# Optimization experiments

Hardware: AMD Instinct MI355X
Metric: run time of the kernel (lower is better)

Reference implementation:

```python
import jax, jax.numpy as jnp
import numpy as np

WS = 7          # window_size
DIM = 256
H = 8           # num_heads
HD = DIM // H   # head_dim = 32
NW = 64         # windows per image
B = 64          # batch of images
B_ = B * NW
M_ = WS * WS + 1  # 50 tokens (cls + patches)


def _relative_position_index():
    coords = np.stack(np.meshgrid(np.arange(WS), np.arange(WS), indexing='ij'))  # (2, ws, ws)
    flat = coords.reshape(2, -1)  # (2, ws*ws)
    rel = flat[:, :, None] - flat[:, None, :]  # (2, N, N)
    rel = rel.transpose(1, 2, 0).astype(np.int64)
    rel[:, :, 0] += WS - 1
    rel[:, :, 1] += WS - 1
    rel[:, :, 0] *= 2 * WS - 1
    return rel.sum(-1).astype(np.int32)  # (N, N) in [0, (2ws-1)^2)


def setup_inputs() -> dict:
    key = jax.random.key(0)
    k1, k2, k3 = jax.random.split(key, 3)
    qkv = jax.random.normal(k1, (B_, M_, 3 * DIM), dtype=jnp.float32)
    mask = jax.random.normal(k2, (NW, M_ - 1, M_), dtype=jnp.float32)
    bias_table = jax.random.normal(k3, ((2 * WS - 1) ** 2, H), dtype=jnp.float32) * 0.02
    rel_index = jnp.asarray(_relative_position_index())
    return {"qkv": qkv, "mask": mask, "bias_table": bias_table, "rel_index": rel_index}


def reference(qkv, mask, bias_table, rel_index):
    Bw, M, C = qkv.shape
    scale = HD ** -0.5
    # (3, B_, H, M, hd)
    qkv = qkv.reshape(Bw, M, 3, H, HD).transpose(2, 0, 3, 1, 4)
    q = qkv[0][:, :, 1:, :] * scale   # queries drop cls token: (B_, H, M-1, hd)
    k, v = qkv[1], qkv[2]             # (B_, H, M, hd)
    attn = jnp.einsum('bhqd,bhkd->bhqk', q, k)  # (B_, H, M-1, M)
    # relative position bias over patch-patch block only
    N = WS * WS
    bias = bias_table[rel_index.reshape(-1)].reshape(N, N, H).transpose(2, 0, 1)  # (H, N, N)
    attn = jnp.concatenate([attn[..., :1], attn[..., 1:] + bias[None]], axis=-1)
    # additive window mask
    nW = mask.shape[0]
    attn = attn.reshape(Bw // nW, nW, H, M - 1, M) + mask[None, :, None]
    attn = jax.nn.softmax(attn.reshape(Bw, H, M - 1, M), axis=-1)
    x = jnp.einsum('bhqk,bhkd->bqhd', attn, v).reshape(Bw, M - 1, DIM)
    return x
```

## Files before the change

kernel.cpp:

```cpp
#include <hip/hip_runtime.h>
#include <stdint.h>

#define NQ 49
#define MT 50
#define NH 8
#define HD 32
#define NW 64
#define BWIN 4096
#define M2TOT (NW*NH*NQ*MT)

typedef __attribute__((ext_vector_type(8))) short short8;
typedef __attribute__((ext_vector_type(4))) float f32x4;

__device__ __forceinline__ uint32_t f2u(float x){ union{float f;uint32_t u;}c; c.f=x; return c.u; }
__device__ __forceinline__ float u2f(uint32_t u){ union{float f;uint32_t u;}c; c.u=u; return c.f; }
__device__ __forceinline__ uint32_t bf16rn(float x){
  uint32_t u = f2u(x);
  return (u + 0x7fffu + ((u >> 16) & 1u)) >> 16;
}
__device__ __forceinline__ void bsplit(float x, uint32_t& hi, uint32_t& lo){
  hi = bf16rn(x);
  lo = bf16rn(x - u2f(hi << 16));
}

__global__ void fuse_mb(const float* __restrict__ mask,
                        const float* __restrict__ bias_table,
                        const int*   __restrict__ rel_index,
                        float* __restrict__ M2)
{
  int idx = blockIdx.x * 256 + threadIdx.x;
  if (idx >= M2TOT) return;
  int j  = idx % MT;
  int t  = idx / MT;
  int i  = t % NQ;
  int t2 = t / NQ;
  int h  = t2 % NH;
  int w  = t2 / NH;
  float v = mask[(w * NQ + i) * MT + j];
  if (j > 0) v += bias_table[rel_index[i * NQ + (j - 1)] * NH + h];
  M2[idx] = v;
}

__global__ __launch_bounds__(128, 4)
void winattn_kernel(const float* __restrict__ qkv,
                    const float* __restrict__ M2,
                    float* __restrict__ out)
{
  __shared__ unsigned short sP[2][64 * 64];

  const int wv   = threadIdx.x >> 6;
  const int lane = threadIdx.x & 63;
  const int ln   = lane & 15;
  const int qd   = lane >> 4;

  const int id = blockIdx.x;
  const int b  = id >> 2;
  const int h  = ((id & 3) << 1) | wv;
  const int w  = b & (NW - 1);

  const float* base = qkv + (size_t)b * (MT * 3 * 256);
  const float scale = 0.17677669529663687f;

  short8 qh[4], ql[4], kh[4], kl[4];
#pragma unroll
  for (int t = 0; t < 4; ++t) {
    int m   = 16 * t + ln;
    int tok = (m < NQ ? m : NQ - 1) + 1;
    const float* p = base + (size_t)tok * 768 + h * HD + qd * 8;
    f32x4 e0 = *(const f32x4*)p;
    f32x4 e1 = *(const f32x4*)(p + 4);
#pragma unroll
    for (int j = 0; j < 8; ++j) {
      float x = (j < 4 ? e0[j] : e1[j - 4]) * scale;
      uint32_t hi, lo; bsplit(x, hi, lo);
      qh[t][j] = (short)(unsigned short)hi;
      ql[t][j] = (short)(unsigned short)lo;
    }
  }
#pragma unroll
  for (int u = 0; u < 4; ++u) {
    int n    = 16 * u + ln;
    int ktok = (n < MT ? n : MT - 1);
    const float* p = base + (size_t)ktok * 768 + 256 + h * HD + qd * 8;
    f32x4 e0 = *(const f32x4*)p;
    f32x4 e1 = *(const f32x4*)(p + 4);
#pragma unroll
    for (int j = 0; j < 8; ++j) {
      float x = (j < 4 ? e0[j] : e1[j - 4]);
      uint32_t hi, lo; bsplit(x, hi, lo);
      kh[u][j] = (short)(unsigned short)hi;
      kl[u][j] = (short)(unsigned short)lo;
    }
  }

  f32x4 S[4][4];
#pragma unroll
  for (int t = 0; t < 4; ++t) {
#pragma unroll
    for (int u = 0; u < 4; ++u) {
      f32x4 a = {0.f, 0.f, 0.f, 0.f};
      a = __builtin_amdgcn_mfma_f32_16x16x32_bf16(qh[t], kh[u], a, 0, 0, 0);
      a = __builtin_amdgcn_mfma_f32_16x16x32_bf16(qh[t], kl[u], a, 0, 0, 0);
      a = __builtin_amdgcn_mfma_f32_16x16x32_bf16(ql[t], kh[u], a, 0, 0, 0);
      S[t][u] = a;
    }
  }

  const float* mrow = M2 + ((size_t)(w * NH + h) * NQ) * MT;
#pragma unroll
  for (int t = 0; t < 4; ++t) {
#pragma unroll
    for (int r = 0; r < 4; ++r) {
      int i = 16 * t + 4 * qd + r;
#pragma unroll
      for (int u = 0; u < 4; ++u) {
        int j = 16 * u + ln;
        if (j >= MT)      S[t][u][r] = -1e30f;
        else if (i < NQ)  S[t][u][r] += mrow[i * MT + j];
      }
    }
  }

  float rsumv[4][4];
#pragma unroll
  for (int t = 0; t < 4; ++t) {
#pragma unroll
    for (int r = 0; r < 4; ++r) {
      float mx = fmaxf(fmaxf(S[t][0][r], S[t][1][r]), fmaxf(S[t][2][r], S[t][3][r]));
#pragma unroll
      for (int s = 1; s < 16; s <<= 1) mx = fmaxf(mx, __shfl_xor(mx, s, 16));
      int m  = 16 * t + 4 * qd + r;
      int m7 = m & 7;
      float sum = 0.f;
#pragma unroll
      for (int u = 0; u < 4; ++u) {
        float p = exp2f((S[t][u][r] - mx) * 1.4426950408889634f);
        sum += p;
        int c = 16 * u + ln;
        int addr = m * 64 + ((((c >> 3) ^ m7) << 3) | (c & 7));
        sP[wv][addr] = (unsigned short)bf16rn(p);
      }
#pragma unroll
      for (int s = 1; s < 16; s <<= 1) sum += __shfl_xor(sum, s, 16);
      rsumv[t][r] = sum;
    }
  }
  __syncthreads();

  short8 vh[2][2], vl[2][2];
#pragma unroll
  for (int kt = 0; kt < 2; ++kt) {
#pragma unroll
    for (int u2 = 0; u2 < 2; ++u2) {
#pragma unroll
      for (int j = 0; j < 8; ++j) {
        int k  = 32 * kt + 8 * qd + j;
        int d  = 16 * u2 + ln;
        int kc = (k < MT ? k : MT - 1);
        float x = base[(size_t)kc * 768 + 512 + h * HD + d];
        if (k >= MT) x = 0.f;
        uint32_t hi, lo; bsplit(x, hi, lo);
        vh[kt][u2][j] = (short)(unsigned short)hi;
        vl[kt][u2][j] = (short)(unsigned short)lo;
      }
    }
  }

  f32x4 O[4][2];
#pragma unroll
  for (int t = 0; t < 4; ++t)
#pragma unroll
    for (int u2 = 0; u2 < 2; ++u2) O[t][u2] = (f32x4){0.f, 0.f, 0.f, 0.f};

#pragma unroll
  for (int kt = 0; kt < 2; ++kt) {
#pragma unroll
    for (int t = 0; t < 4; ++t) {
      int m = 16 * t + ln;
      int phys = ((4 * kt + qd) ^ (ln & 7));
      short8 ph = *(const short8*)&sP[wv][m * 64 + (phys << 3)];
#pragma unroll
      for (int u2 = 0; u2 < 2; ++u2) {
        f32x4 a = O[t][u2];
        a = __builtin_amdgcn_mfma_f32_16x16x32_bf16(ph, vh[kt][u2], a, 0, 0, 0);
        a = __builtin_amdgcn_mfma_f32_16x16x32_bf16(ph, vl[kt][u2], a, 0, 0, 0);
        O[t][u2] = a;
      }
    }
  }

#pragma unroll
  for (int t = 0; t < 4; ++t) {
#pragma unroll
    for (int r = 0; r < 4; ++r) {
      int row = 16 * t + 4 * qd + r;
      if (row >= NQ) continue;
      float inv = 1.0f / rsumv[t][r];
#pragma unroll
      for (int u2 = 0; u2 < 2; ++u2) {
        int d = 16 * u2 + ln;
        out[(((size_t)b * NQ + row) * NH + h) * HD + d] = O[t][u2][r] * inv;
      }
    }
  }
}

extern "C" void kernel_launch(void* const* d_in, const int* in_sizes, int n_in,
                              void* d_out, int out_size, void* d_ws, size_t ws_size,
                              hipStream_t stream) {
  (void)in_sizes; (void)n_in; (void)ws_size; (void)out_size;
  const float* qkv        = (const float*)d_in[0];
  const float* mask       = (const float*)d_in[1];
  const float* bias_table = (const float*)d_in[2];
  const int*   rel_index  = (const int*)d_in[3];
  float* out = (float*)d_out;
  float* M2  = (float*)d_ws;

  fuse_mb<<<(M2TOT + 255) / 256, 256, 0, stream>>>(mask, bias_table, rel_index, M2);
  winattn_kernel<<<BWIN * 4, 128, 0, stream>>>(qkv, M2, out);
}
```

Baseline: 944.6 us.

## Fuse mask+bias precompute into attention kernel and stream Q tiles per row block

Drops the separate fuse_mb kernel and its M2 workspace. The attention kernel now reads the mask and gathers the relative-position bias directly through rel_index and bias_table. Q tiles are loaded and split per row block inside the score loop, which cuts live registers for Q and S. The hi part of the bf16 split now truncates instead of rounding. This removes a launch and the M2 write/read traffic, but adds an indirect gather per score element and changes the split rounding slightly.

```diff
diff --git a/kernel.cpp b/kernel.cpp
--- a/kernel.cpp
+++ b/kernel.cpp
@@ -7,7 +7,6 @@
 #define HD 32
 #define NW 64
 #define BWIN 4096
-#define M2TOT (NW*NH*NQ*MT)
 
 typedef __attribute__((ext_vector_type(8))) short short8;
 typedef __attribute__((ext_vector_type(4))) float f32x4;
@@ -19,31 +18,16 @@
   return (u + 0x7fffu + ((u >> 16) & 1u)) >> 16;
 }
 __device__ __forceinline__ void bsplit(float x, uint32_t& hi, uint32_t& lo){
-  hi = bf16rn(x);
-  lo = bf16rn(x - u2f(hi << 16));
-}
-
-__global__ void fuse_mb(const float* __restrict__ mask,
-                        const float* __restrict__ bias_table,
-                        const int*   __restrict__ rel_index,
-                        float* __restrict__ M2)
-{
-  int idx = blockIdx.x * 256 + threadIdx.x;
-  if (idx >= M2TOT) return;
-  int j  = idx % MT;
-  int t  = idx / MT;
-  int i  = t % NQ;
-  int t2 = t / NQ;
-  int h  = t2 % NH;
-  int w  = t2 / NH;
-  float v = mask[(w * NQ + i) * MT + j];
-  if (j > 0) v += bias_table[rel_index[i * NQ + (j - 1)] * NH + h];
-  M2[idx] = v;
+  uint32_t u = f2u(x);
+  hi = u >> 16;
+  lo = bf16rn(x - u2f(u & 0xffff0000u));
 }
 
 __global__ __launch_bounds__(128, 4)
 void winattn_kernel(const float* __restrict__ qkv,
-                    const float* __restrict__ M2,
+                    const float* __restrict__ mask,
+                    const float* __restrict__ bias_table,
+                    const int*   __restrict__ rel_index,
                     float* __restrict__ out)
 {
   __shared__ unsigned short sP[2][64 * 64];
@@ -61,22 +45,7 @@
   const float* base = qkv + (size_t)b * (MT * 3 * 256);
   const float scale = 0.17677669529663687f;
 
-  short8 qh[4], ql[4], kh[4], kl[4];
-#pragma unroll
-  for (int t = 0; t < 4; ++t) {
-    int m   = 16 * t + ln;
-    int tok = (m < NQ ? m : NQ - 1) + 1;
-    const float* p = base + (size_t)tok * 768 + h * HD + qd * 8;
-    f32x4 e0 = *(const f32x4*)p;
-    f32x4 e1 = *(const f32x4*)(p + 4);
-#pragma unroll
-    for (int j = 0; j < 8; ++j) {
-      float x = (j < 4 ? e0[j] : e1[j - 4]) * scale;
-      uint32_t hi, lo; bsplit(x, hi, lo);
-      qh[t][j] = (short)(unsigned short)hi;
-      ql[t][j] = (short)(unsigned short)lo;
-    }
-  }
+  short8 kh[4], kl[4];
 #pragma unroll
   for (int u = 0; u < 4; ++u) {
     int n    = 16 * u + ln;
@@ -93,52 +62,61 @@
     }
   }
 
-  f32x4 S[4][4];
+  const float* mrow = mask + (size_t)w * NQ * MT;
+  float rsumv[4][4];
+
 #pragma unroll
   for (int t = 0; t < 4; ++t) {
+    int m   = 16 * t + ln;
+    int tok = (m < NQ ? m : NQ - 1) + 1;
+    const float* p = base + (size_t)tok * 768 + h * HD + qd * 8;
+    f32x4 e0 = *(const f32x4*)p;
+    f32x4 e1 = *(const f32x4*)(p + 4);
+    short8 qh, ql;
+#pragma unroll
+    for (int j = 0; j < 8; ++j) {
+      float x = (j < 4 ? e0[j] : e1[j - 4]) * scale;
+      uint32_t hi, lo; bsplit(x, hi, lo);
+      qh[j] = (short)(unsigned short)hi;
+      ql[j] = (short)(unsigned short)lo;
+    }
+
+    f32x4 S[4];
 #pragma unroll
     for (int u = 0; u < 4; ++u) {
       f32x4 a = {0.f, 0.f, 0.f, 0.f};
-      a = __builtin_amdgcn_mfma_f32_16x16x32_bf16(qh[t], kh[u], a, 0, 0, 0);
-      a = __builtin_amdgcn_mfma_f32_16x16x32_bf16(qh[t], kl[u], a, 0, 0, 0);
-      a = __builtin_amdgcn_mfma_f32_16x16x32_bf16(ql[t], kh[u], a, 0, 0, 0);
-      S[t][u] = a;
+      a = __builtin_amdgcn_mfma_f32_16x16x32_bf16(qh, kh[u], a, 0, 0, 0);
+      a = __builtin_amdgcn_mfma_f32_16x16x32_bf16(qh, kl[u], a, 0, 0, 0);
+      a = __builtin_amdgcn_mfma_f32_16x16x32_bf16(ql, kh[u], a, 0, 0, 0);
+      S[u] = a;
     }
-  }
 
-  const float* mrow = M2 + ((size_t)(w * NH + h) * NQ) * MT;
-#pragma unroll
-  for (int t = 0; t < 4; ++t) {
 #pragma unroll
     for (int r = 0; r < 4; ++r) {
       int i = 16 * t + 4 * qd + r;
 #pragma unroll
       for (int u = 0; u < 4; ++u) {
         int j = 16 * u + ln;
-        if (j >= MT)      S[t][u][r] = -1e30f;
-        else if (i < NQ)  S[t][u][r] += mrow[i * MT + j];
+        if (j >= MT)      S[u][r] = -1e30f;
+        else if (i < NQ) {
+          float add = mrow[i * MT + j];
+          if (j > 0)
+            add += bias_table[rel_index[i * NQ + (j - 1)] * NH + h];
+          S[u][r] += add;
+        }
       }
-    }
-  }
-
-  float rsumv[4][4];
-#pragma unroll
-  for (int t = 0; t < 4; ++t) {
-#pragma unroll
-    for (int r = 0; r < 4; ++r) {
-      float mx = fmaxf(fmaxf(S[t][0][r], S[t][1][r]), fmaxf(S[t][2][r], S[t][3][r]));
+      float mx = fmaxf(fmaxf(S[0][r], S[1][r]), fmaxf(S[2][r], S[3][r]));
 #pragma unroll
       for (int s = 1; s < 16; s <<= 1) mx = fmaxf(mx, __shfl_xor(mx, s, 16));
-      int m  = 16 * t + 4 * qd + r;
-      int m7 = m & 7;
+      int m7 = i & 7;
       float sum = 0.f;
 #pragma unroll
       for (int u = 0; u < 4; ++u) {
-        float p = exp2f((S[t][u][r] - mx) * 1.4426950408889634f);
-        sum += p;
+        float pv = exp2f((S[u][r] - mx) * 1.4426950408889634f);
+        sum += pv;
         int c = 16 * u + ln;
-        int addr = m * 64 + ((((c >> 3) ^ m7) << 3) | (c & 7));
-        sP[wv][addr] = (unsigned short)bf16rn(p);
+        int addr = i * 64 + ((((c >> 3) ^ m7) << 3) | (c & 7));
+        sP[wv][addr] = (unsigned short)bf16rn(pv);
       }
 #pragma unroll
       for (int s = 1; s < 16; s <<= 1) sum += __shfl_xor(sum, s, 16);
@@ -208,14 +186,12 @@
 extern "C" void kernel_launch(void* const* d_in, const int* in_sizes, int n_in,
                               void* d_out, int out_size, void* d_ws, size_t ws_size,
                               hipStream_t stream) {
-  (void)in_sizes; (void)n_in; (void)ws_size; (void)out_size;
+  (void)in_sizes; (void)n_in; (void)ws_size; (void)out_size; (void)d_ws;
   const float* qkv        = (const float*)d_in[0];
   const float* mask       = (const float*)d_in[1];
   const float* bias_table = (const float*)d_in[2];
   const int*   rel_index  = (const int*)d_in[3];
   float* out = (float*)d_out;
-  float* M2  = (float*)d_ws;
 
-  fuse_mb<<<(M2TOT + 255) / 256, 256, 0, stream>>>(mask, bias_table, rel_index, M2);
-  winattn_kernel<<<BWIN * 4, 128, 0, stream>>>(qkv, M2, out);
+  winattn_kernel<<<BWIN * 4, 128, 0, stream>>>(qkv, mask, bias_table, rel_index, out);
 }
```

New measurement: 1.026 ms. 1.09x slower.
